# Kernel optimization log

Hardware: AMD Instinct MI355X
Metric: run time of the kernel (lower is better)

## Reference

```python
import jax, jax.numpy as jnp
import numpy as np

N, M, D = 8192, 8192, 128
EPS = 1e-9


def setup_inputs() -> dict:
    key = jax.random.key(0)
    k1, k2 = jax.random.split(key)
    X = jax.random.normal(k1, (N, D), dtype=jnp.float32)
    Y = jax.random.normal(k2, (M, D), dtype=jnp.float32)
    sigma = jnp.ones((1,), dtype=jnp.float32)  # bandwidth (self.sigma)
    return {"X": X, "Y": Y, "sigma": sigma}


def reference(X, Y, sigma):
    # l2norm: ||x_i - y_j||^2 = ||x_i||^2 - 2 x_i.y_j + ||y_j||^2
    # (original builds full XX/YY Gram matrices just for their diagonals;
    #  same math via row-wise sums of squares)
    x2 = jnp.sum(X * X, axis=1)          # [n]
    y2 = jnp.sum(Y * Y, axis=1)          # [m]
    xy = jnp.matmul(X, Y.T)              # [n, m]
    dnorm2 = x2[:, None] - 2.0 * xy + y2[None, :]
    sigma2_inv = 1.0 / (sigma[0] ** 2 + EPS)
    K_XY = jnp.exp(-sigma2_inv * dnorm2)  # [n, m]
    return K_XY
```

## Files before the change

### kernel.cpp

```cpp
#include <hip/hip_runtime.h>
#include <stdint.h>

#define D_DIM 128
#define NROW 8192
#define MROW 8192
#define OUT_LD 8192
#define LDP 136
#define BAND 16
#define CTILE 128
#define NTILE (MROW / CTILE)

typedef __bf16 bf16x8 __attribute__((ext_vector_type(8)));
typedef float f32x4 __attribute__((ext_vector_type(4)));
typedef unsigned short us8 __attribute__((ext_vector_type(8)));

__global__ __launch_bounds__(256) void rbf_prep(const float* __restrict__ X,
                                                const float* __restrict__ Y,
                                                float* __restrict__ nrm,
                                                unsigned short* __restrict__ Xb,
                                                unsigned short* __restrict__ Yb) {
    const int t = threadIdx.x;
    const int w = t >> 6, lane = t & 63;
    const int rid = blockIdx.x * 4 + w;
    const float* src;
    unsigned short* dst;
    if (rid < NROW) { src = X + (size_t)rid * D_DIM;          dst = Xb + (size_t)rid * D_DIM; }
    else            { src = Y + (size_t)(rid - NROW) * D_DIM; dst = Yb + (size_t)(rid - NROW) * D_DIM; }
    float2 v = *(const float2*)(src + 2 * lane);
    union { __bf16 h[2]; uint32_t u; } cv;
    cv.h[0] = (__bf16)v.x; cv.h[1] = (__bf16)v.y;
    *(uint32_t*)(dst + 2 * lane) = cv.u;
    float s = v.x * v.x + v.y * v.y;
    #pragma unroll
    for (int off = 32; off > 0; off >>= 1) s += __shfl_xor(s, off, 64);
    if (lane == 0) nrm[rid] = s;
}

__global__ __launch_bounds__(256, 2) void rbf_band(const unsigned short* __restrict__ Xb,
                                                   const unsigned short* __restrict__ Yb,
                                                   const float* __restrict__ sigma,
                                                   const float* __restrict__ nrm,
                                                   float* __restrict__ out) {
    __shared__ __align__(16) unsigned short Ys[2][CTILE][LDP];
    __shared__ __align__(16) unsigned short Xs[BAND][LDP];

    const int t = threadIdx.x;
    const int w = t >> 6, ln = t & 63;
    const int quad = ln >> 4, l16 = ln & 15;
    const int row0 = blockIdx.x * BAND;
    const int yw = w * 32;

    {
        int r = t >> 4, k = (t & 15) * 8;
        *(us8*)(&Xs[r][k]) = *(const us8*)(Xb + (size_t)(row0 + r) * D_DIM + k);
    }

    auto stageY = [&](int ct, int buf) {
        #pragma unroll
        for (int i = 0; i < 8; ++i) {
            int f = t + 256 * i;
            int r = f >> 4;
            int k = (f & 15) * 8;
            *(us8*)(&Ys[buf][r][k]) = *(const us8*)(Yb + (size_t)(ct * CTILE + r) * D_DIM + k);
        }
    };

    stageY(0, 0);
    __syncthreads();

    const float x2 = nrm[row0 + l16];
    const float s2 = sigma[0] * sigma[0] + 1e-9f;
    const float cexp = -1.4426950408889634f / s2;
    float* orow = out + (size_t)(row0 + l16) * OUT_LD;

    for (int ct = 0; ct < NTILE; ++ct) {
        const int cur = ct & 1;
        if (ct < NTILE - 1) stageY(ct + 1, cur ^ 1);

        f32x4 acc[2] = {};
        #pragma unroll
        for (int ks = 0; ks < 4; ++ks) {
            const int k = ks * 32 + quad * 8;
            bf16x8 b = *(const bf16x8*)(&Xs[l16][k]);
            #pragma unroll
            for (int tj = 0; tj < 2; ++tj) {
                bf16x8 a = *(const bf16x8*)(&Ys[cur][yw + tj * 16 + l16][k]);
                acc[tj] = __builtin_amdgcn_mfma_f32_16x16x32_bf16(a, b, acc[tj], 0, 0, 0);
            }
        }

        #pragma unroll
        for (int tj = 0; tj < 2; ++tj) {
            const int colb = ct * CTILE + yw + tj * 16 + quad * 4;
            f32x4 y2v = *(const f32x4*)(nrm + NROW + colb);
            f32x4 v;
            #pragma unroll
            for (int r = 0; r < 4; ++r) {
                float d = x2 + y2v[r] - 2.0f * acc[tj][r];
                v[r] = __builtin_amdgcn_exp2f(d * cexp);
            }
            __builtin_nontemporal_store(v, (f32x4*)(orow + colb));
        }
        __syncthreads();
    }
}

extern "C" void kernel_launch(void* const* d_in, const int* in_sizes, int n_in,
                              void* d_out, int out_size, void* d_ws, size_t ws_size,
                              hipStream_t stream) {
    const float* X = (const float*)d_in[0];
    const float* Y = (const float*)d_in[1];
    const float* sigma = (const float*)d_in[2];
    float* nrm = (float*)d_ws;
    unsigned short* Xb = (unsigned short*)d_ws + 32768;
    unsigned short* Yb = Xb + (size_t)NROW * D_DIM;
    float* out = (float*)d_out;

    rbf_prep<<<(NROW + MROW) / 4, 256, 0, stream>>>(X, Y, nrm, Xb, Yb);
    rbf_band<<<NROW / BAND, 256, 0, stream>>>(Xb, Yb, sigma, nrm, out);
}
```

Before: 314.1 us.

## Retile RBF kernel into 128x128 output tiles with register-resident X fragments

```diff
diff --git a/kernel.cpp b/kernel.cpp
--- a/kernel.cpp
+++ b/kernel.cpp
@@ -6,9 +6,9 @@
 #define MROW 8192
 #define OUT_LD 8192
 #define LDP 136
-#define BAND 16
+#define PANEL 1024
 #define CTILE 128
-#define NTILE (MROW / CTILE)
+#define NT_PER_BLK (PANEL / CTILE)
 
 typedef __bf16 bf16x8 __attribute__((ext_vector_type(8)));
 typedef float f32x4 __attribute__((ext_vector_type(4)));
@@ -41,67 +41,78 @@
                                                    const float* __restrict__ sigma,
                                                    const float* __restrict__ nrm,
                                                    float* __restrict__ out) {
-    __shared__ __align__(16) unsigned short Ys[2][CTILE][LDP];
-    __shared__ __align__(16) unsigned short Xs[BAND][LDP];
+    __shared__ __align__(16) unsigned short Ys[CTILE][LDP];
+
+    const int b = blockIdx.x;
+    const int panel = b & 7;
+    const int row0 = (b >> 3) * 128;
+    const int pcol0 = panel * PANEL;
 
     const int t = threadIdx.x;
     const int w = t >> 6, ln = t & 63;
     const int quad = ln >> 4, l16 = ln & 15;
-    const int row0 = blockIdx.x * BAND;
-    const int yw = w * 32;
+    const int wr = (w >> 1) * 64;
+    const int wc = (w & 1) * 64;
 
-    {
-        int r = t >> 4, k = (t & 15) * 8;
-        *(us8*)(&Xs[r][k]) = *(const us8*)(Xb + (size_t)(row0 + r) * D_DIM + k);
-    }
+    bf16x8 xf[4][4];
+    #pragma unroll
+    for (int ti = 0; ti < 4; ++ti)
+        #pragma unroll
+        for (int ks = 0; ks < 4; ++ks)
+            xf[ti][ks] = *(const bf16x8*)(Xb + (size_t)(row0 + wr + ti * 16 + l16) * D_DIM
+                                          + ks * 32 + quad * 8);
 
-    auto stageY = [&](int ct, int buf) {
+    const float s2 = sigma[0] * sigma[0] + 1e-9f;
+    const float cexp = -1.4426950408889634f / s2;
+    const float c2 = -2.0f * cexp;
+
+    float x2c[4];
+    #pragma unroll
+    for (int ti = 0; ti < 4; ++ti)
+        x2c[ti] = nrm[row0 + wr + ti * 16 + l16] * cexp;
+
+    for (int ct = 0; ct < NT_PER_BLK; ++ct) {
+        const int col0 = pcol0 + ct * CTILE;
+        if (ct > 0) __syncthreads();
+
         #pragma unroll
         for (int i = 0; i < 8; ++i) {
             int f = t + 256 * i;
             int r = f >> 4;
             int k = (f & 15) * 8;
-            *(us8*)(&Ys[buf][r][k]) = *(const us8*)(Yb + (size_t)(ct * CTILE + r) * D_DIM + k);
+            *(us8*)(&Ys[r][k]) = *(const us8*)(Yb + (size_t)(col0 + r) * D_DIM + k);
         }
-    };
+        __syncthreads();
 
-    stageY(0, 0);
-    __syncthreads();
-
-    const float x2 = nrm[row0 + l16];
-    const float s2 = sigma[0] * sigma[0] + 1e-9f;
-    const float cexp = -1.4426950408889634f / s2;
-    float* orow = out + (size_t)(row0 + l16) * OUT_LD;
-
-    for (int ct = 0; ct < NTILE; ++ct) {
-        const int cur = ct & 1;
-        if (ct < NTILE - 1) stageY(ct + 1, cur ^ 1);
-
-        f32x4 acc[2] = {};
+        f32x4 acc[4][4] = {};
         #pragma unroll
         for (int ks = 0; ks < 4; ++ks) {
             const int k = ks * 32 + quad * 8;
-            bf16x8 b = *(const bf16x8*)(&Xs[l16][k]);
+            bf16x8 yf[4];
             #pragma unroll
-            for (int tj = 0; tj < 2; ++tj) {
-                bf16x8 a = *(const bf16x8*)(&Ys[cur][yw + tj * 16 + l16][k]);
-                acc[tj] = __builtin_amdgcn_mfma_f32_16x16x32_bf16(a, b, acc[tj], 0, 0, 0);
-            }
+            for (int tj = 0; tj < 4; ++tj)
+                yf[tj] = *(const bf16x8*)(&Ys[wc + tj * 16 + l16][k]);
+            #pragma unroll
+            for (int ti = 0; ti < 4; ++ti)
+                #pragma unroll
+                for (int tj = 0; tj < 4; ++tj)
+                    acc[ti][tj] = __builtin_amdgcn_mfma_f32_16x16x32_bf16(yf[tj], xf[ti][ks], acc[ti][tj], 0, 0, 0);
         }
 
         #pragma unroll
-        for (int tj = 0; tj < 2; ++tj) {
-            const int colb = ct * CTILE + yw + tj * 16 + quad * 4;
-            f32x4 y2v = *(const f32x4*)(nrm + NROW + colb);
-            f32x4 v;
+        for (int ti = 0; ti < 4; ++ti) {
+            const size_t grow = (size_t)(row0 + wr + ti * 16 + l16);
             #pragma unroll
-            for (int r = 0; r < 4; ++r) {
-                float d = x2 + y2v[r] - 2.0f * acc[tj][r];
-                v[r] = __builtin_amdgcn_exp2f(d * cexp);
+            for (int tj = 0; tj < 4; ++tj) {
+                const int colb = col0 + wc + tj * 16 + quad * 4;
+                f32x4 y2v = *(const f32x4*)(nrm + NROW + colb);
+                f32x4 v;
+                #pragma unroll
+                for (int r = 0; r < 4; ++r)
+                    v[r] = __builtin_amdgcn_exp2f(fmaf(c2, acc[ti][tj][r], x2c[ti] + y2v[r] * cexp));
+                __builtin_nontemporal_store(v, (f32x4*)(out + grow * OUT_LD + colb));
             }
-            __builtin_nontemporal_store(v, (f32x4*)(orow + colb));
         }
-        __syncthreads();
     }
 }
 
@@ -117,5 +128,5 @@
     float* out = (float*)d_out;
 
     rbf_prep<<<(NROW + MROW) / 4, 256, 0, stream>>>(X, Y, nrm, Xb, Yb);
-    rbf_band<<<NROW / BAND, 256, 0, stream>>>(Xb, Yb, sigma, nrm, out);
+    rbf_band<<<(NROW / 128) * 8, 256, 0, stream>>>(Xb, Yb, sigma, nrm, out);
 }
```

Measured after the change: 342.2 us. 1.09x slower.
